# Kernel tuning notes

Measured on AMD Instinct MI355X. Metric: run time of the kernel, lower is better.

Reference implementation:

```python
import jax, jax.numpy as jnp
import numpy as np
from jax.scipy.special import erf

N_NODES = 128
LAMBDA_MAX = 0.06
EPS = 1e-7


def normal_cdf(x):
    # standard normal CDF, mu=0 sigma2=1
    return 0.5 * (1.0 + erf(x / jnp.sqrt(jnp.asarray(2.0, x.dtype))))


def construct_trajectory(d, c, a, n_nodes):
    """d: [S, N-1], c: [S, N-2], a: [S, N-2, N-1] -> x: [S, N, N-1].

    Sequential recurrence: at each node, QR-orthogonalize the acceleration
    against the previous heading, rotate the heading by angle c, and step by
    distance d. Implemented as lax.scan over nodes (strictly sequential).
    """
    S = d.shape[0]
    D = n_nodes - 1  # effective dim
    e0 = jnp.zeros((S, D), dtype=d.dtype).at[:, 0].set(1.0)  # v_h at node 1
    x1 = d[:, :1] * e0  # x at node 1 (node 0 is origin)

    def step(carry, inp):
        v_prev, x_prev = carry            # [S, D], [S, D]
        a_i, c_i, d_i = inp               # [S, D], [S], [S]
        M = jnp.stack([v_prev, a_i], axis=-1)     # [S, D, 2]
        Q, _ = jnp.linalg.qr(M)                   # batched thin QR
        a_orth = Q[..., 1]                        # orthonormal accel direction
        v = jnp.cos(c_i)[:, None] * v_prev + jnp.sin(c_i)[:, None] * a_orth
        x_new = x_prev + d_i[:, None] * v
        return (v, x_new), x_new

    xs = (jnp.moveaxis(a, 1, 0), c.T, d[:, 1:].T)  # leading axis = N-2 steps
    (_, _), x_rest = jax.lax.scan(step, (e0, x1), xs)  # x_rest: [N-2, S, D]

    x = jnp.concatenate(
        [jnp.zeros((S, 1, D), dtype=d.dtype), x1[:, None, :],
         jnp.moveaxis(x_rest, 0, 1)], axis=1)
    return x  # [S, N, D]


def pairwise_dists(x):
    # x: [S, N, D] -> [S, N, N], via the gram-matrix trick (no [S,N,N,D] blowup)
    sq = jnp.sum(x * x, axis=-1)                         # [S, N]
    gram = jnp.einsum('snd,smd->snm', x, x)              # [S, N, N]
    d2 = sq[:, :, None] + sq[:, None, :] - 2.0 * gram
    return jnp.sqrt(jnp.maximum(d2, 0.0))


def reference(d_raw, c_raw, a_raw, l_raw, all_trials, correct_trials):
    # transforms
    d = jax.nn.softplus(d_raw)                 # rectifier
    c = c_raw                                  # identity
    a = a_raw                                  # identity (orthonormalized later)
    lapse = LAMBDA_MAX * normal_cdf(l_raw)     # [S, 1]

    x = construct_trajectory(d, c, a, N_NODES)         # [S, N, N-1]
    pdists = pairwise_dists(x)                         # [S, N, N]

    sqrt2 = jnp.sqrt(jnp.asarray(2.0, pdists.dtype))
    p_axb = (normal_cdf(pdists / sqrt2) * normal_cdf(pdists / 2.0)
             + normal_cdf(-pdists / sqrt2) * normal_cdf(-pdists / 2.0))
    lam = lapse[:, :, None]                            # [S, 1, 1]
    probs = (1.0 - 2.0 * lam) * p_axb + lam
    probs = jnp.clip(probs, EPS, 1.0 - EPS)

    n_all = all_trials.astype(probs.dtype)[None, :, :]
    n_cor = correct_trials.astype(probs.dtype)[None, :, :]
    ll = n_cor * jnp.log(probs) + (n_all - n_cor) * jnp.log1p(-probs)
    # sum over node pairs, Monte-Carlo mean over samples
    return jnp.mean(jnp.sum(ll, axis=(1, 2)))


def setup_inputs() -> dict:
    key = jax.random.key(0)
    k1, k2, k3, k4, k5, k6 = jax.random.split(key, 6)
    S, N = 2048, N_NODES
    return {
        'd_raw': jax.random.normal(k1, (S, N - 1), dtype=jnp.float32),
        'c_raw': jax.random.normal(k2, (S, N - 2), dtype=jnp.float32),
        'a_raw': jax.random.normal(k3, (S, N - 2, N - 1), dtype=jnp.float32),
        'l_raw': jax.random.normal(k4, (S, 1), dtype=jnp.float32),
        'all_trials': jax.random.randint(k5, (N, N), 0, 80, dtype=jnp.int32),
        'correct_trials': jax.random.randint(k6, (N, N), 0, 40, dtype=jnp.int32),
    }
```

## Files before the change

### kernel.cpp

```cpp
#include <hip/hip_runtime.h>
#include <math.h>

#define S_TOT   2048
#define NNODES  128
#define D_DIM   127
#define N_STEPS 126

typedef unsigned short ushort_t;
typedef unsigned int   uint_t;
typedef __attribute__((ext_vector_type(8))) short bfrag;
typedef __attribute__((ext_vector_type(4))) float f4;

__device__ __forceinline__ float softplus_f(float x) {
    return log1pf(expf(-fabsf(x))) + fmaxf(x, 0.0f);
}
__device__ __forceinline__ float normal_cdf_f(float x) {
    return 0.5f * (1.0f + erff(x * 0.7071067811865475f));
}
__device__ __forceinline__ float frl(float x, int lane) {
    return __int_as_float(__builtin_amdgcn_readlane(__float_as_int(x), lane));
}
__device__ __forceinline__ float wave_sum(float x) {
    float r = x; int v;
    v = __builtin_amdgcn_update_dpp(0, __float_as_int(r), 0x111, 0xf, 0xf, true); r += __int_as_float(v);
    v = __builtin_amdgcn_update_dpp(0, __float_as_int(r), 0x112, 0xf, 0xf, true); r += __int_as_float(v);
    v = __builtin_amdgcn_update_dpp(0, __float_as_int(r), 0x114, 0xf, 0xf, true); r += __int_as_float(v);
    v = __builtin_amdgcn_update_dpp(0, __float_as_int(r), 0x118, 0xf, 0xf, true); r += __int_as_float(v);
    v = __builtin_amdgcn_update_dpp(0, __float_as_int(r), 0x142, 0xa, 0xf, true); r += __int_as_float(v);
    v = __builtin_amdgcn_update_dpp(0, __float_as_int(r), 0x143, 0xc, 0xf, true); r += __int_as_float(v);
    return frl(r, 63);
}
__device__ __forceinline__ ushort_t f2bf(float x) {
    uint_t u = __float_as_uint(x);
    uint_t r = u + 0x7fffu + ((u >> 16) & 1u);
    return (ushort_t)(r >> 16);
}
__device__ __forceinline__ float bf2f(ushort_t h) {
    return __uint_as_float(((uint_t)h) << 16);
}

__global__ __launch_bounds__(256) void prep_counts(
        const int* __restrict__ all_t, const int* __restrict__ cor_t,
        uint_t* __restrict__ pk) {
    int i = blockIdx.x * 256 + threadIdx.x;
    int n = i >> 7, m = i & 127;
    int at = all_t[i], ct = cor_t[i];
    if (n != m) { at += all_t[m * 128 + n]; ct += cor_t[m * 128 + n]; }
    pk[i] = (uint_t)f2bf((float)ct) | ((uint_t)f2bf((float)(at - ct)) << 16);
}

#define LDR1(A, B, row)                                                       \
    { const float* _p = ap + (size_t)(row) * D_DIM + 2 * lane;                \
      A = _p[0];                                                              \
      float _t = _p[d1ok ? 1 : 0];                \
      B = d1ok ? _t : 0.0f; }

#define LOAD_G(BASE, GUARD)                                                   \
    { const int _b = (BASE); const bool _gd = (GUARD);                        \
      if (!_gd || _b + 0  < 126) LDR1(sa0,  sb0,  _b + 0)  else { sa0 = 0; sb0 = 0; }   \
      if (!_gd || _b + 1  < 126) LDR1(sa1,  sb1,  _b + 1)  else { sa1 = 0; sb1 = 0; }   \
      if (!_gd || _b + 2  < 126) LDR1(sa2,  sb2,  _b + 2)  else { sa2 = 0; sb2 = 0; }   \
      if (!_gd || _b + 3  < 126) LDR1(sa3,  sb3,  _b + 3)  else { sa3 = 0; sb3 = 0; }   \
      if (!_gd || _b + 4  < 126) LDR1(sa4,  sb4,  _b + 4)  else { sa4 = 0; sb4 = 0; }   \
      if (!_gd || _b + 5  < 126) LDR1(sa5,  sb5,  _b + 5)  else { sa5 = 0; sb5 = 0; }   \
      if (!_gd || _b + 6  < 126) LDR1(sa6,  sb6,  _b + 6)  else { sa6 = 0; sb6 = 0; }   \
      if (!_gd || _b + 7  < 126) LDR1(sa7,  sb7,  _b + 7)  else { sa7 = 0; sb7 = 0; }   \
      if (!_gd || _b + 8  < 126) LDR1(sa8,  sb8,  _b + 8)  else { sa8 = 0; sb8 = 0; }   \
      if (!_gd || _b + 9  < 126) LDR1(sa9,  sb9,  _b + 9)  else { sa9 = 0; sb9 = 0; }   \
      if (!_gd || _b + 10 < 126) LDR1(sa10, sb10, _b + 10) else { sa10 = 0; sb10 = 0; } \
      if (!_gd || _b + 11 < 126) LDR1(sa11, sb11, _b + 11) else { sa11 = 0; sb11 = 0; } \
      if (!_gd || _b + 12 < 126) LDR1(sa12, sb12, _b + 12) else { sa12 = 0; sb12 = 0; } \
      if (!_gd || _b + 13 < 126) LDR1(sa13, sb13, _b + 13) else { sa13 = 0; sb13 = 0; } \
      if (!_gd || _b + 14 < 126) LDR1(sa14, sb14, _b + 14) else { sa14 = 0; sb14 = 0; } \
      if (!_gd || _b + 15 < 126) LDR1(sa15, sb15, _b + 15) else { sa15 = 0; sb15 = 0; } }

#define WRITE_G(SB)                                                           \
    { const int _s = (SB);                                                    \
      *(float2*)&abuf[_s + 0 ][2 * lane] = make_float2(sa0,  sb0);            \
      *(float2*)&abuf[_s + 1 ][2 * lane] = make_float2(sa1,  sb1);            \
      *(float2*)&abuf[_s + 2 ][2 * lane] = make_float2(sa2,  sb2);            \
      *(float2*)&abuf[_s + 3 ][2 * lane] = make_float2(sa3,  sb3);            \
      *(float2*)&abuf[_s + 4 ][2 * lane] = make_float2(sa4,  sb4);            \
      *(float2*)&abuf[_s + 5 ][2 * lane] = make_float2(sa5,  sb5);            \
      *(float2*)&abuf[_s + 6 ][2 * lane] = make_float2(sa6,  sb6);            \
      *(float2*)&abuf[_s + 7 ][2 * lane] = make_float2(sa7,  sb7);            \
      *(float2*)&abuf[_s + 8 ][2 * lane] = make_float2(sa8,  sb8);            \
      *(float2*)&abuf[_s + 9 ][2 * lane] = make_float2(sa9,  sb9);            \
      *(float2*)&abuf[_s + 10][2 * lane] = make_float2(sa10, sb10);           \
      *(float2*)&abuf[_s + 11][2 * lane] = make_float2(sa11, sb11);           \
      *(float2*)&abuf[_s + 12][2 * lane] = make_float2(sa12, sb12);           \
      *(float2*)&abuf[_s + 13][2 * lane] = make_float2(sa13, sb13);           \
      *(float2*)&abuf[_s + 14][2 * lane] = make_float2(sa14, sb14);           \
      *(float2*)&abuf[_s + 15][2 * lane] = make_float2(sa15, sb15); }

#define STEP_CORE(I, SC, SA, SR, ROWRD, CLSI, DLSI, FLUSH)                    \
    {                                                                         \
        const float ca = ra_r[SC], cb = rb_r[SC];                             \
        float va = wave_sum(fmaf(v0, ca, v1 * cb));                           \
        float ua = fmaf(fmaf(-vp0, aE0U, va), rcp_v, aE0U);                   \
        float w1 = fmaf(-ua, vp1s, aE1U);                                     \
        float inv = __builtin_amdgcn_rsqf(fmaf(-va, va, aaU));                \
        float invs = (w1 >= 0.0f) ? -inv : inv;                               \
        float sf = sU * invs;                                                 \
        float nv0 = fmaf(cU, v0, sf * fmaf(-va, v0, ca));                     \
        float nv1 = fmaf(cU, v1, sf * fmaf(-va, v1, cb));                     \
        float np0 = fmaf(cU, vp0, sf * fmaf(-va, vp0, aE0U));                 \
        float np1 = fmaf(cU, vp1, sf * fmaf(-va, vp1, aE1U));                 \
        v0 = nv0; v1 = nv1; vp0 = np0; vp1 = np1;                             \
        { float ns = copysignf(1.0f, vp0);                                    \
          rcp_v = __builtin_amdgcn_rcpf(vp0 + ns); vp1s = vp1 * ns; }         \
        x0 = fmaf(dU, v0, x0); x1 = fmaf(dU, v1, x1);                         \
        { uint_t pk;                                                          \
          asm("v_cvt_pk_bf16_f32 %0, %1, %2" : "=v"(pk) : "v"(x0), "v"(x1));  \
          xstage[(((I) + 2) & 7) * 64 + lane] = pk; }    \
        aaU = aa1; aE0U = aE0_1; aE1U = aE1_1; cU = c1; sU = s1; dU = d1;     \
        aa1 = wave_sum(fmaf(ra_r[SA], ra_r[SA], rb_r[SA] * rb_r[SA]));        \
        aE0_1 = frl(ra_r[SA], 0); aE1_1 = frl(rb_r[SA], 0);                   \
        { float2 cs = cls2[CLSI]; c1 = cs.x; s1 = cs.y; }                     \
        d1 = dls[DLSI];                                                       \
        { float2 nx = *(float2*)&abuf[ROWRD][2 * lane];                       \
          ra_r[SR] = nx.x; rb_r[SR] = nx.y; }                                 \
        if (FLUSH) {        \
            uint4 t0 = *(uint4*)&xstage[4 * lane];                            \
            uint4 t1 = *(uint4*)&xstage[256 + 4 * lane];                      \
            uint_t* dst = xg + ((I) - 5) * 64;                                \
            *(uint4*)(dst + 4 * lane) = t0;                                   \
            *(uint4*)(dst + 256 + 4 * lane) = t1;                             \
        }                                                                     \
    }

#define MSTEP(J) STEP_CORE(ib + (J), (J) & 3, ((J) + 2) & 3, ((J) + 3) & 3,   \
                           (ib + (J) + 3) & 31, ib + (J) + 2, ib + (J) + 3,   \
                           ((J) == 5 || (J) == 13))
#define TSTEP(J) STEP_CORE(112 + (J), (J) & 3, ((J) + 2) & 3, ((J) + 3) & 3,  \
                           ((115 + (J) < 125) ? (115 + (J)) : 125) & 31,      \
                           ((114 + (J) < 127) ? (114 + (J)) : 127),           \
                           ((115 + (J) < 127) ? (115 + (J)) : 127),           \
                           ((J) == 5 || (J) == 13))

__global__
__attribute__((amdgpu_flat_work_group_size(64, 64), amdgpu_waves_per_eu(2, 2)))
void traj_kernel(
        const float* __restrict__ d_raw, const float* __restrict__ c_raw,
        const float* __restrict__ a_raw,
        uint_t* __restrict__ xout, int s_base) {
    const int li = blockIdx.x;
    const int s  = s_base + li;
    const int lane = threadIdx.x;
    const bool d1ok = lane < 63;

    __shared__ __align__(16) float abuf[32][128];
    __shared__ __align__(16) uint_t xstage[512];
    __shared__ float  dls[128];
    __shared__ float2 cls2[128];

    float t0 = softplus_f(d_raw[(size_t)s * D_DIM + lane]);
    dls[lane] = t0;
    dls[64 + lane] = d1ok ? softplus_f(d_raw[(size_t)s * D_DIM + 64 + lane]) : 0.0f;
    {
        float cv = c_raw[(size_t)s * N_STEPS + lane];
        cls2[lane] = make_float2(__cosf(cv), __sinf(cv));
        if (lane < 62) {
            float cv2 = c_raw[(size_t)s * N_STEPS + 64 + lane];
            cls2[64 + lane] = make_float2(__cosf(cv2), __sinf(cv2));
        } else {
            cls2[64 + lane] = make_float2(0.0f, 0.0f);
        }
    }

    const float* ap = a_raw + (size_t)s * N_STEPS * D_DIM;
    uint_t* xg = xout + (size_t)li * NNODES * 64;

    float sa0, sa1, sa2, sa3, sa4, sa5, sa6, sa7,
          sa8, sa9, sa10, sa11, sa12, sa13, sa14, sa15;
    float sb0, sb1, sb2, sb3, sb4, sb5, sb6, sb7,
          sb8, sb9, sb10, sb11, sb12, sb13, sb14, sb15;

    LOAD_G(0, false)  WRITE_G(0)
    LOAD_G(16, false) WRITE_G(16)
    LOAD_G(32, false)

    float ra_r[4], rb_r[4];
    { float2 t = *(float2*)&abuf[0][2 * lane]; ra_r[0] = t.x; rb_r[0] = t.y; }
    { float2 t = *(float2*)&abuf[1][2 * lane]; ra_r[1] = t.x; rb_r[1] = t.y; }
    { float2 t = *(float2*)&abuf[2][2 * lane]; ra_r[2] = t.x; rb_r[2] = t.y; }
    ra_r[3] = 0.0f; rb_r[3] = 0.0f;
    float aaU = wave_sum(fmaf(ra_r[0], ra_r[0], rb_r[0] * rb_r[0]));
    float aa1 = wave_sum(fmaf(ra_r[1], ra_r[1], rb_r[1] * rb_r[1]));
    float aE0U = frl(ra_r[0], 0), aE1U = frl(rb_r[0], 0);
    float aE0_1 = frl(ra_r[1], 0), aE1_1 = frl(rb_r[1], 0);
    float cU, sU, c1, s1;
    { float2 cs = cls2[0]; cU = cs.x; sU = cs.y; }
    { float2 cs = cls2[1]; c1 = cs.x; s1 = cs.y; }
    float dU = dls[1], d1 = dls[2];

    float v0 = (lane == 0) ? 1.0f : 0.0f, v1 = 0.0f;
    float vp0 = 1.0f, vp1 = 0.0f, vp1s = 0.0f, rcp_v = 0.5f;
    float x0 = (lane == 0) ? t0 : 0.0f, x1 = 0.0f;

    xstage[lane] = 0u;
    {
        uint_t pk0;
        asm("v_cvt_pk_bf16_f32 %0, %1, %2" : "=v"(pk0) : "v"(x0), "v"(x1));
        xstage[64 + lane] = pk0;
    }

    #pragma unroll 1
    for (int g = 0; g < 7; ++g) {
        const int ib = g << 4;
        MSTEP(0)  MSTEP(1)  MSTEP(2)  MSTEP(3)
        MSTEP(4)  MSTEP(5)  MSTEP(6)  MSTEP(7)
        MSTEP(8)  MSTEP(9)  MSTEP(10) MSTEP(11)
        MSTEP(12) MSTEP(13) MSTEP(14) MSTEP(15)
        if (g <= 5) { WRITE_G((g & 1) << 4) }
        if (g <= 4) LOAD_G((g + 3) << 4, g == 4)
    }
    TSTEP(0)  TSTEP(1)  TSTEP(2)  TSTEP(3)
    TSTEP(4)  TSTEP(5)  TSTEP(6)  TSTEP(7)
    TSTEP(8)  TSTEP(9)  TSTEP(10) TSTEP(11)
    TSTEP(12) TSTEP(13)
}
#undef MSTEP
#undef TSTEP
#undef STEP_CORE
#undef LOAD_G
#undef WRITE_G
#undef LDR1

__device__ __forceinline__ bfrag ldfrag(const ushort_t* base, int row, int kelem) {
    int byte = ((row << 8) + (kelem << 1)) ^ ((row & 7) << 4);
    return *(const bfrag*)((const char*)base + byte);
}

template<int W>
__device__ __forceinline__ void gram_w(const ushort_t* Xs, f4 (&acc)[9],
                                       int lr, int lg) {
    constexpr int RA = W, RB = 7 - W;
    #pragma unroll
    for (int ks = 0; ks < 4; ++ks) {
        const int kb = ks * 32 + lg * 8;
        const bfrag ha = ldfrag(Xs, RA * 16 + lr, kb);
        const bfrag hb = ldfrag(Xs, RB * 16 + lr, kb);
        #pragma unroll
        for (int TC = W; TC < 8; ++TC) {
            const bfrag bh = ldfrag(Xs, TC * 16 + lr, kb);
            acc[TC - W] = __builtin_amdgcn_mfma_f32_16x16x32_bf16(ha, bh, acc[TC - W], 0, 0, 0);
            if (TC >= RB)
                acc[TC + 1] = __builtin_amdgcn_mfma_f32_16x16x32_bf16(hb, bh, acc[TC + 1], 0, 0, 0);
        }
    }
}

template<int W>
__device__ __forceinline__ void write_sq(const f4 (&acc)[9], float* sq, int lr, int lg) {
    #pragma unroll
    for (int q = 0; q < 4; ++q) {
        if (4 * lg + q == lr) {
            sq[W * 16 + lr]       = acc[0][q];
            sq[(7 - W) * 16 + lr] = acc[8 - W][q];
        }
    }
}

__device__ __forceinline__ float entry_ll(float g, float sqn, float sqm,
        uint_t cw, float lam, float one_m2l) {
    const float d2 = fmaxf(sqn + sqm - 2.0f * g, 0.0f);
    const float pd = __builtin_amdgcn_sqrtf(d2);
    const float A = 0.344f, B = 5.334f, IA = 0.656f, C = 0.3989422804f;
    const float z1 = 0.70710678f * pd, z2 = 0.5f * pd;
    const float e1 = __expf(-0.25f  * d2) * C;
    const float e2 = __expf(-0.125f * d2) * C;
    const float den1 = fmaf(A, __builtin_amdgcn_sqrtf(fmaf(0.5f,  d2, B)), IA * z1);
    const float den2 = fmaf(A, __builtin_amdgcn_sqrtf(fmaf(0.25f, d2, B)), IA * z2);
    const float F1 = e1 * __builtin_amdgcn_rcpf(den1);
    const float F2 = e2 * __builtin_amdgcn_rcpf(den2);
    const float qax = F1 + F2 - 2.0f * F1 * F2;
    float qp = fmaf(one_m2l, qax, lam);
    qp = fminf(fmaxf(qp, 1e-7f), 1.0f - 1e-7f);
    const float pp = 1.0f - qp;
    const float c   = bf2f((ushort_t)(cw & 0xffffu));
    const float amc = bf2f((ushort_t)(cw >> 16));
    return c * __logf(pp) + amc * __logf(qp);
}

__device__ __forceinline__ float tile_ll(f4 a, int TR, int TC, bool diag,
        int lr, int lg, const float* sq, const uint_t* __restrict__ cnt,
        float lam, float one_m2l) {
    float s = 0.0f;
    #pragma unroll
    for (int q = 0; q < 4; ++q) {
        const int n = TR * 16 + 4 * lg + q;
        const int m = TC * 16 + lr;
        if (!diag || (4 * lg + q) <= lr)
            s += entry_ll(a[q], sq[n], sq[m], cnt[n * 128 + m], lam, one_m2l);
    }
    return s;
}

template<int W>
__device__ __forceinline__ float epi(const f4 (&acc)[9], const float* sq,
        const uint_t* __restrict__ cnt, int lr, int lg, float lam, float one_m2l) {
    constexpr int RA = W, RB = 7 - W;
    float s = 0.0f;
    #pragma unroll
    for (int TC = W; TC < 8; ++TC) {
        s += tile_ll(acc[TC - W], RA, TC, (TC == RA), lr, lg, sq, cnt, lam, one_m2l);
        if (TC >= RB)
            s += tile_ll(acc[TC + 1], RB, TC, (TC == RB), lr, lg, sq, cnt, lam, one_m2l);
    }
    return s;
}

__global__ __launch_bounds__(256, 4) void ll_kernel(
        const uint_t* __restrict__ x_g,
        const float* __restrict__ l_raw, const uint_t* __restrict__ cnt,
        float* __restrict__ sums, int s_base) {
    const int li = blockIdx.x;
    const int s  = s_base + li;
    const int t  = threadIdx.x;

    __shared__ __align__(16) ushort_t Xs[NNODES * 128];
    __shared__ float sq[NNODES];
    __shared__ float wsum[4];

    const uint_t* gx = x_g + (size_t)li * NNODES * 64;
    const int l = t & 63, w = t >> 6, lr = l & 15, lg = l >> 4;

    #pragma unroll
    for (int ii = 0; ii < 8; ++ii) {
        const int i = t + ii * 256;
        const int row = i >> 4, j = i & 15;
        const uint4 v = *(const uint4*)(gx + row * 64 + j * 4);
        const int b = ((row << 8) + (j << 4)) ^ ((row & 7) << 4);
        *(uint4*)((char*)Xs + b) = v;
    }
    __syncthreads();

    f4 acc[9];
    #pragma unroll
    for (int i = 0; i < 9; ++i) acc[i] = (f4)(0.0f);

    switch (w) {
        case 0: gram_w<0>(Xs, acc, lr, lg); write_sq<0>(acc, sq, lr, lg); break;
        case 1: gram_w<1>(Xs, acc, lr, lg); write_sq<1>(acc, sq, lr, lg); break;
        case 2: gram_w<2>(Xs, acc, lr, lg); write_sq<2>(acc, sq, lr, lg); break;
        default: gram_w<3>(Xs, acc, lr, lg); write_sq<3>(acc, sq, lr, lg); break;
    }
    __syncthreads();

    const float lam = 0.06f * normal_cdf_f(l_raw[s]);
    const float one_m2l = 1.0f - 2.0f * lam;
    float ll = 0.0f;
    switch (w) {
        case 0: ll = epi<0>(acc, sq, cnt, lr, lg, lam, one_m2l); break;
        case 1: ll = epi<1>(acc, sq, cnt, lr, lg, lam, one_m2l); break;
        case 2: ll = epi<2>(acc, sq, cnt, lr, lg, lam, one_m2l); break;
        default: ll = epi<3>(acc, sq, cnt, lr, lg, lam, one_m2l); break;
    }

    const float wtot = wave_sum(ll);
    if (l == 0) wsum[w] = wtot;
    __syncthreads();
    if (t == 0) sums[s] = wsum[0] + wsum[1] + wsum[2] + wsum[3];
}

__global__ __launch_bounds__(256) void reduce_kernel(
        const float* __restrict__ sums, float* __restrict__ out) {
    __shared__ double sh[256];
    const int t = threadIdx.x;
    double acc = 0.0;
    for (int i = t; i < S_TOT; i += 256) acc += (double)sums[i];
    sh[t] = acc;
    __syncthreads();
    for (int off = 128; off > 0; off >>= 1) {
        if (t < off) sh[t] += sh[t + off];
        __syncthreads();
    }
    if (t == 0) out[0] = (float)(sh[0] / (double)S_TOT);
}

extern "C" void kernel_launch(void* const* d_in, const int* in_sizes, int n_in,
                              void* d_out, int out_size, void* d_ws, size_t ws_size,
                              hipStream_t stream) {
    (void)in_sizes; (void)n_in; (void)out_size;
    const float* d_raw = (const float*)d_in[0];
    const float* c_raw = (const float*)d_in[1];
    const float* a_raw = (const float*)d_in[2];
    const float* l_raw = (const float*)d_in[3];
    const int*   all_t = (const int*)d_in[4];
    const int*   cor_t = (const int*)d_in[5];
    float* out = (float*)d_out;

    char*   ws   = (char*)d_ws;
    float*  sums = (float*)ws;
    uint_t* cnt  = (uint_t*)(ws + 8192);
    char*   xbase = ws + 8192 + 65536;
    const size_t per_sample = (size_t)NNODES * 64 * sizeof(uint_t);

    const size_t head = 8192 + 65536;
    size_t avail = (ws_size > head) ? ws_size - head : 0;
    int chunk = (int)(avail / per_sample);
    if (chunk > S_TOT) chunk = S_TOT;
    if (chunk < 1) chunk = 1;

    prep_counts<<<64, 256, 0, stream>>>(all_t, cor_t, cnt);

    for (int s0 = 0; s0 < S_TOT; s0 += chunk) {
        const int nblk = (S_TOT - s0 < chunk) ? (S_TOT - s0) : chunk;
        uint_t* xbuf = (uint_t*)xbase;
        traj_kernel<<<nblk, 64, 0, stream>>>(d_raw, c_raw, a_raw, xbuf, s0);
        ll_kernel<<<nblk, 256, 0, stream>>>(xbuf, l_raw, cnt, sums, s0);
    }
    reduce_kernel<<<1, 256, 0, stream>>>(sums, out);
}
```

Baseline: 101.0 us.

## Process recurrence steps in pairs with a batched dual wave reduction

The sequential trajectory recurrence now advances two nodes per iteration. It algebraically expresses the second step's projection v·a_{i+1} via the first step's coefficients and a precomputed Gram term a_i·a_{i+1}, so both dot products share one interleaved DPP reduction. This shortens the serial cross-lane reduction chain on the critical path, roughly halving dependent reductions per node. In exchange it adds more registers (an 8-slot ring), a 3-way reduction for the norms and the Gram term, and slightly different floating-point rounding.

```diff
diff --git a/kernel.cpp b/kernel.cpp
--- a/kernel.cpp
+++ b/kernel.cpp
@@ -29,6 +29,28 @@
     v = __builtin_amdgcn_update_dpp(0, __float_as_int(r), 0x142, 0xa, 0xf, true); r += __int_as_float(v);
     v = __builtin_amdgcn_update_dpp(0, __float_as_int(r), 0x143, 0xc, 0xf, true); r += __int_as_float(v);
     return frl(r, 63);
+}
+__device__ __forceinline__ void wave_sum2(float a, float b, float& ra, float& rb) {
+    float x = a, y = b; int v;
+#define STG2(C, RM)                                                            \
+    v = __builtin_amdgcn_update_dpp(0, __float_as_int(x), C, RM, 0xf, true); x += __int_as_float(v); \
+    v = __builtin_amdgcn_update_dpp(0, __float_as_int(y), C, RM, 0xf, true); y += __int_as_float(v);
+    STG2(0x111, 0xf) STG2(0x112, 0xf) STG2(0x114, 0xf)
+    STG2(0x118, 0xf) STG2(0x142, 0xa) STG2(0x143, 0xc)
+#undef STG2
+    ra = frl(x, 63); rb = frl(y, 63);
+}
+__device__ __forceinline__ void wave_sum3(float a, float b, float c,
+                                          float& ra, float& rb, float& rc) {
+    float x = a, y = b, z = c; int v;
+#define STG3(C, RM)                                                            \
+    v = __builtin_amdgcn_update_dpp(0, __float_as_int(x), C, RM, 0xf, true); x += __int_as_float(v); \
+    v = __builtin_amdgcn_update_dpp(0, __float_as_int(y), C, RM, 0xf, true); y += __int_as_float(v); \
+    v = __builtin_amdgcn_update_dpp(0, __float_as_int(z), C, RM, 0xf, true); z += __int_as_float(v);
+    STG3(0x111, 0xf) STG3(0x112, 0xf) STG3(0x114, 0xf)
+    STG3(0x118, 0xf) STG3(0x142, 0xa) STG3(0x143, 0xc)
+#undef STG3
+    ra = frl(x, 63); rb = frl(y, 63); rc = frl(z, 63);
 }
 __device__ __forceinline__ ushort_t f2bf(float x) {
     uint_t u = __float_as_uint(x);
@@ -93,50 +115,91 @@
       *(float2*)&abuf[_s + 14][2 * lane] = make_float2(sa14, sb14);           \
       *(float2*)&abuf[_s + 15][2 * lane] = make_float2(sa15, sb15); }
 
-#define STEP_CORE(I, SC, SA, SR, ROWRD, CLSI, DLSI, FLUSH)                    \
+#define RD_RING(SL, ROW)                                                      \
+    { float2 t = *(float2*)&abuf[(ROW) & 31][2 * lane];                       \
+      raR[SL] = t.x; rbR[SL] = t.y; }
+
+#define PAIR_CORE(S0, S1, S2, S3, S4, S5, S6, S7, R6, R7, TI0, TI1, TD0, TD1, \
+                  FLUSH, FROW)                                                \
     {                                                                         \
-        const float ca = ra_r[SC], cb = rb_r[SC];                             \
-        float va = wave_sum(fmaf(v0, ca, v1 * cb));                           \
-        float ua = fmaf(fmaf(-vp0, aE0U, va), rcp_v, aE0U);                   \
-        float w1 = fmaf(-ua, vp1s, aE1U);                                     \
-        float inv = __builtin_amdgcn_rsqf(fmaf(-va, va, aaU));                \
-        float invs = (w1 >= 0.0f) ? -inv : inv;                               \
-        float sf = sU * invs;                                                 \
-        float nv0 = fmaf(cU, v0, sf * fmaf(-va, v0, ca));                     \
-        float nv1 = fmaf(cU, v1, sf * fmaf(-va, v1, cb));                     \
-        float np0 = fmaf(cU, vp0, sf * fmaf(-va, vp0, aE0U));                 \
-        float np1 = fmaf(cU, vp1, sf * fmaf(-va, vp1, aE1U));                 \
-        v0 = nv0; v1 = nv1; vp0 = np0; vp1 = np1;                             \
-        { float ns = copysignf(1.0f, vp0);                                    \
-          rcp_v = __builtin_amdgcn_rcpf(vp0 + ns); vp1s = vp1 * ns; }         \
-        x0 = fmaf(dU, v0, x0); x1 = fmaf(dU, v1, x1);                         \
+                  \
+        float m0 = fmaf(v0, raR[S0], v1 * rbR[S0]);                           \
+        float m1 = fmaf(v0, raR[S1], v1 * rbR[S1]);                           \
+        float r0, r1; wave_sum2(m0, m1, r0, r1);                              \
+        const float va0 = r0;                                                 \
+        float ua0 = fmaf(fmaf(-V0, aE00, va0), rcp_v, aE00);                  \
+        float w10 = fmaf(-ua0, V1s, aE01);                                    \
+        float iv0 = __builtin_amdgcn_rsqf(fmaf(-va0, va0, aaU0));             \
+        float sf0 = s0u * ((w10 >= 0.0f) ? -iv0 : iv0);                       \
+        float al0 = fmaf(-sf0, va0, c0u), be0 = sf0;                          \
+        float V0a = fmaf(al0, V0, be0 * aE00);                                \
+        float V1a = fmaf(al0, V1, be0 * aE01);                                \
+        float sg1 = copysignf(1.0f, V0a);                                     \
+        float rv1 = __builtin_amdgcn_rcpf(V0a + sg1);                         \
+        float V1as = V1a * sg1;                                               \
+        float va1 = fmaf(al0, r1, be0 * gU);                                  \
+        float ua1 = fmaf(fmaf(-V0a, aE10, va1), rv1, aE10);                   \
+        float w11 = fmaf(-ua1, V1as, aE11);                                   \
+        float iv1 = __builtin_amdgcn_rsqf(fmaf(-va1, va1, aaU1));             \
+        float sf1 = s1u * ((w11 >= 0.0f) ? -iv1 : iv1);                       \
+        float al1 = fmaf(-sf1, va1, c1u), be1 = sf1;                          \
+        V0 = fmaf(al1, V0a, be1 * aE10);                                      \
+        V1 = fmaf(al1, V1a, be1 * aE11);                                      \
+        { float sg = copysignf(1.0f, V0);                                     \
+          rcp_v = __builtin_amdgcn_rcpf(V0 + sg); V1s = V1 * sg; }            \
+                                                 \
+        float w0a = fmaf(al0, v0, be0 * raR[S0]);                             \
+        float w1a = fmaf(al0, v1, be0 * rbR[S0]);                             \
+        v0 = fmaf(al1, w0a, be1 * raR[S1]);                                   \
+        v1 = fmaf(al1, w1a, be1 * rbR[S1]);                                   \
+        x0 = fmaf(d0u, w0a, x0); x1 = fmaf(d0u, w1a, x1);                     \
         { uint_t pk;                                                          \
           asm("v_cvt_pk_bf16_f32 %0, %1, %2" : "=v"(pk) : "v"(x0), "v"(x1));  \
-          xstage[(((I) + 2) & 7) * 64 + lane] = pk; }    \
-        aaU = aa1; aE0U = aE0_1; aE1U = aE1_1; cU = c1; sU = s1; dU = d1;     \
-        aa1 = wave_sum(fmaf(ra_r[SA], ra_r[SA], rb_r[SA] * rb_r[SA]));        \
-        aE0_1 = frl(ra_r[SA], 0); aE1_1 = frl(rb_r[SA], 0);                   \
-        { float2 cs = cls2[CLSI]; c1 = cs.x; s1 = cs.y; }                     \
-        d1 = dls[DLSI];                                                       \
-        { float2 nx = *(float2*)&abuf[ROWRD][2 * lane];                       \
-          ra_r[SR] = nx.x; rb_r[SR] = nx.y; }                                 \
-        if (FLUSH) {        \
+          xstage[(S2) * 64 + lane] = pk; }                                    \
+        x0 = fmaf(d1u, v0, x0); x1 = fmaf(d1u, v1, x1);                       \
+        { uint_t pk;                                                          \
+          asm("v_cvt_pk_bf16_f32 %0, %1, %2" : "=v"(pk) : "v"(x0), "v"(x1));  \
+          xstage[(S3) * 64 + lane] = pk; }                                    \
+                                                  \
+        aaU0 = aaN0; aaU1 = aaN1; gU = gN;                                    \
+        aE00 = aE00N; aE01 = aE01N; aE10 = aE10N; aE11 = aE11N;               \
+        c0u = c0N; s0u = s0N; c1u = c1N; s1u = s1N; d0u = d0N; d1u = d1N;     \
+           \
+        { float p0 = fmaf(raR[S4], raR[S4], rbR[S4] * rbR[S4]);               \
+          float p1 = fmaf(raR[S5], raR[S5], rbR[S5] * rbR[S5]);               \
+          float p2 = fmaf(raR[S4], raR[S5], rbR[S4] * rbR[S5]);               \
+          wave_sum3(p0, p1, p2, aaN0, aaN1, gN); }                            \
+        aE00N = frl(raR[S4], 0); aE01N = frl(rbR[S4], 0);                     \
+        aE10N = frl(raR[S5], 0); aE11N = frl(rbR[S5], 0);                     \
+        { float2 cs = cls2[TI0]; c0N = cs.x; s0N = cs.y; }                    \
+        { float2 cs = cls2[TI1]; c1N = cs.x; s1N = cs.y; }                    \
+        d0N = dls[TD0]; d1N = dls[TD1];                                       \
+        RD_RING(S6, R6)                                                       \
+        RD_RING(S7, R7)                                                       \
+        if (FLUSH) {                                                          \
             uint4 t0 = *(uint4*)&xstage[4 * lane];                            \
             uint4 t1 = *(uint4*)&xstage[256 + 4 * lane];                      \
-            uint_t* dst = xg + ((I) - 5) * 64;                                \
+            uint_t* dst = xg + (FROW) * 64;                                   \
             *(uint4*)(dst + 4 * lane) = t0;                                   \
             *(uint4*)(dst + 256 + 4 * lane) = t1;                             \
         }                                                                     \
     }
 
-#define MSTEP(J) STEP_CORE(ib + (J), (J) & 3, ((J) + 2) & 3, ((J) + 3) & 3,   \
-                           (ib + (J) + 3) & 31, ib + (J) + 2, ib + (J) + 3,   \
-                           ((J) == 5 || (J) == 13))
-#define TSTEP(J) STEP_CORE(112 + (J), (J) & 3, ((J) + 2) & 3, ((J) + 3) & 3,  \
-                           ((115 + (J) < 125) ? (115 + (J)) : 125) & 31,      \
-                           ((114 + (J) < 127) ? (114 + (J)) : 127),           \
-                           ((115 + (J) < 127) ? (115 + (J)) : 127),           \
-                           ((J) == 5 || (J) == 13))
+#define MPAIR(J) PAIR_CORE((2*(J)) & 7, (2*(J)+1) & 7, (2*(J)+2) & 7,         \
+                           (2*(J)+3) & 7, (2*(J)+4) & 7, (2*(J)+5) & 7,       \
+                           (2*(J)+6) & 7, (2*(J)+7) & 7,                      \
+                           ibp + 2*(J) + 6, ibp + 2*(J) + 7,                  \
+                           ibp + 2*(J) + 4, ibp + 2*(J) + 5,                  \
+                           ibp + 2*(J) + 5, ibp + 2*(J) + 6,                  \
+                           ((J) == 2 || (J) == 6), ibp + 2*(J) - 4)
+#define TCL(V, M) (((V) < (M)) ? (V) : (M))
+#define TPAIR(J) PAIR_CORE((2*(J)) & 7, (2*(J)+1) & 7, (2*(J)+2) & 7,         \
+                           (2*(J)+3) & 7, (2*(J)+4) & 7, (2*(J)+5) & 7,       \
+                           (2*(J)+6) & 7, (2*(J)+7) & 7,                      \
+                           TCL(112 + 2*(J) + 6, 125), TCL(112 + 2*(J) + 7, 125), \
+                           TCL(112 + 2*(J) + 4, 127), TCL(112 + 2*(J) + 5, 127), \
+                           TCL(112 + 2*(J) + 5, 127), TCL(112 + 2*(J) + 6, 127), \
+                           ((J) == 2 || (J) == 6), 112 + 2*(J) - 4)
 
 __global__
 __attribute__((amdgpu_flat_work_group_size(64, 64), amdgpu_waves_per_eu(2, 2)))
@@ -180,22 +243,37 @@
     LOAD_G(16, false) WRITE_G(16)
     LOAD_G(32, false)
 
-    float ra_r[4], rb_r[4];
-    { float2 t = *(float2*)&abuf[0][2 * lane]; ra_r[0] = t.x; rb_r[0] = t.y; }
-    { float2 t = *(float2*)&abuf[1][2 * lane]; ra_r[1] = t.x; rb_r[1] = t.y; }
-    { float2 t = *(float2*)&abuf[2][2 * lane]; ra_r[2] = t.x; rb_r[2] = t.y; }
-    ra_r[3] = 0.0f; rb_r[3] = 0.0f;
-    float aaU = wave_sum(fmaf(ra_r[0], ra_r[0], rb_r[0] * rb_r[0]));
-    float aa1 = wave_sum(fmaf(ra_r[1], ra_r[1], rb_r[1] * rb_r[1]));
-    float aE0U = frl(ra_r[0], 0), aE1U = frl(rb_r[0], 0);
-    float aE0_1 = frl(ra_r[1], 0), aE1_1 = frl(rb_r[1], 0);
-    float cU, sU, c1, s1;
-    { float2 cs = cls2[0]; cU = cs.x; sU = cs.y; }
-    { float2 cs = cls2[1]; c1 = cs.x; s1 = cs.y; }
-    float dU = dls[1], d1 = dls[2];
+    float raR[8], rbR[8];
+    RD_RING(0, 0) RD_RING(1, 1) RD_RING(2, 2)
+    RD_RING(3, 3) RD_RING(4, 4) RD_RING(5, 5)
+    raR[6] = 0.0f; rbR[6] = 0.0f; raR[7] = 0.0f; rbR[7] = 0.0f;
+
+    float aaU0, aaU1, gU, aaN0, aaN1, gN;
+    {
+        float p0 = fmaf(raR[0], raR[0], rbR[0] * rbR[0]);
+        float p1 = fmaf(raR[1], raR[1], rbR[1] * rbR[1]);
+        float p2 = fmaf(raR[0], raR[1], rbR[0] * rbR[1]);
+        wave_sum3(p0, p1, p2, aaU0, aaU1, gU);
+    }
+    {
+        float p0 = fmaf(raR[2], raR[2], rbR[2] * rbR[2]);
+        float p1 = fmaf(raR[3], raR[3], rbR[3] * rbR[3]);
+        float p2 = fmaf(raR[2], raR[3], rbR[2] * rbR[3]);
+        wave_sum3(p0, p1, p2, aaN0, aaN1, gN);
+    }
+    float aE00 = frl(raR[0], 0), aE01 = frl(rbR[0], 0);
+    float aE10 = frl(raR[1], 0), aE11 = frl(rbR[1], 0);
+    float aE00N = frl(raR[2], 0), aE01N = frl(rbR[2], 0);
+    float aE10N = frl(raR[3], 0), aE11N = frl(rbR[3], 0);
+    float c0u, s0u, c1u, s1u, c0N, s0N, c1N, s1N;
+    { float2 cs = cls2[0]; c0u = cs.x; s0u = cs.y; }
+    { float2 cs = cls2[1]; c1u = cs.x; s1u = cs.y; }
+    { float2 cs = cls2[2]; c0N = cs.x; s0N = cs.y; }
+    { float2 cs = cls2[3]; c1N = cs.x; s1N = cs.y; }
+    float d0u = dls[1], d1u = dls[2], d0N = dls[3], d1N = dls[4];
 
     float v0 = (lane == 0) ? 1.0f : 0.0f, v1 = 0.0f;
-    float vp0 = 1.0f, vp1 = 0.0f, vp1s = 0.0f, rcp_v = 0.5f;
+    float V0 = 1.0f, V1 = 0.0f, V1s = 0.0f, rcp_v = 0.5f;
     float x0 = (lane == 0) ? t0 : 0.0f, x1 = 0.0f;
 
     xstage[lane] = 0u;
@@ -207,22 +285,20 @@
 
     #pragma unroll 1
     for (int g = 0; g < 7; ++g) {
-        const int ib = g << 4;
-        MSTEP(0)  MSTEP(1)  MSTEP(2)  MSTEP(3)
-        MSTEP(4)  MSTEP(5)  MSTEP(6)  MSTEP(7)
-        MSTEP(8)  MSTEP(9)  MSTEP(10) MSTEP(11)
-        MSTEP(12) MSTEP(13) MSTEP(14) MSTEP(15)
+        const int ibp = g << 4;
+        MPAIR(0) MPAIR(1) MPAIR(2) MPAIR(3)
+        MPAIR(4) MPAIR(5) MPAIR(6) MPAIR(7)
         if (g <= 5) { WRITE_G((g & 1) << 4) }
         if (g <= 4) LOAD_G((g + 3) << 4, g == 4)
     }
-    TSTEP(0)  TSTEP(1)  TSTEP(2)  TSTEP(3)
-    TSTEP(4)  TSTEP(5)  TSTEP(6)  TSTEP(7)
-    TSTEP(8)  TSTEP(9)  TSTEP(10) TSTEP(11)
-    TSTEP(12) TSTEP(13)
-}
-#undef MSTEP
-#undef TSTEP
-#undef STEP_CORE
+    TPAIR(0) TPAIR(1) TPAIR(2) TPAIR(3)
+    TPAIR(4) TPAIR(5) TPAIR(6)
+}
+#undef MPAIR
+#undef TPAIR
+#undef TCL
+#undef PAIR_CORE
+#undef RD_RING
 #undef LOAD_G
 #undef WRITE_G
 #undef LDR1
```

After: 100.6 us. About the same (-0.4%).
